# Kernel optimization log

Hardware: AMD Instinct MI355X
Metric: run time of the kernel (lower is better)

The kernel has to match this reference:

```python
import jax, jax.numpy as jnp
import numpy as np

B, S, D, NB = 64, 2048, 512, 8
MAX_BLOCK = 64  # block lengths drawn from [1, MAX_BLOCK)


def setup_inputs() -> dict:
    key = jax.random.key(0)
    k_h, k_c, k_w, k_len, k_sel = jax.random.split(key, 5)
    h = jax.random.normal(k_h, (B, D), dtype=jnp.float32)
    context = jax.random.normal(k_c, (B, S, D), dtype=jnp.float32)
    W = jax.random.normal(k_w, (D, D), dtype=jnp.float32) / np.sqrt(D)
    # block lengths >= 1 so the selected block softmax is never empty;
    # sum of all blocks + 1 <= NB*(MAX_BLOCK-1)+1 < S, so slices stay in range
    sub_seq_lengths = jax.random.randint(k_len, (B, NB), 1, MAX_BLOCK, dtype=jnp.int32)
    selected_block_idx = jax.random.randint(k_sel, (B,), 0, NB, dtype=jnp.int32)
    return {"h": h, "context": context, "W": W,
            "sub_seq_lengths": sub_seq_lengths,
            "selected_block_idx": selected_block_idx}


def reference(h, context, W, sub_seq_lengths, selected_block_idx):
    # attn[b,s] = context[b,s] . (W h[b])   (linear_in has no bias)
    target = h @ W.T                                  # [B, D]
    attn = jnp.einsum('bsd,bd->bs', context, target)  # [B, S]

    # per-sample selected-block boundaries: sc = sum(lengths[:idx]) + 1
    starts = jnp.cumsum(sub_seq_lengths, axis=1) - sub_seq_lengths  # exclusive cumsum [B, NB]
    b = jnp.arange(h.shape[0])
    sc = starts[b, selected_block_idx] + 1            # [B]
    L = sub_seq_lengths[b, selected_block_idx]        # [B]

    pos = jnp.arange(context.shape[1])[None, :]       # [1, S]
    in_block = (pos >= sc[:, None]) & (pos < (sc + L)[:, None])  # [B, S]

    # masked softmax restricted to the selected block (vectorized over batch)
    p = jax.nn.softmax(jnp.where(in_block, attn, -jnp.inf), axis=1)
    p = jnp.where(in_block, p, 0.0)
    weighted_context = jnp.einsum('bs,bsd->bd', p, context)  # [B, D]
    return weighted_context, attn
```

## Files before the change

### kernel.cpp

```cpp
#include <hip/hip_runtime.h>
#include <hip/hip_bf16.h>
#include <stdint.h>

#define BB   64
#define SS   2048
#define DD   512
#define NBLK 8

typedef unsigned short u16;
typedef unsigned int   u32;

__device__ __forceinline__ float lo2f(u32 u) {
    union { u32 i; float f; } v; v.i = u << 16; return v.f;
}
__device__ __forceinline__ float hi2f(u32 u) {
    union { u32 i; float f; } v; v.i = u & 0xffff0000u; return v.f;
}

template<bool BF16>
__device__ __forceinline__ void load8(const void* base, size_t off, float* o) {
    if (BF16) {
        const uint4 v = *(const uint4*)((const u16*)base + off);
        o[0]=lo2f(v.x); o[1]=hi2f(v.x); o[2]=lo2f(v.y); o[3]=hi2f(v.y);
        o[4]=lo2f(v.z); o[5]=hi2f(v.z); o[6]=lo2f(v.w); o[7]=hi2f(v.w);
    } else {
        const float4* p = (const float4*)((const float*)base + off);
        const float4 a = p[0], b = p[1];
        o[0]=a.x; o[1]=a.y; o[2]=a.z; o[3]=a.w;
        o[4]=b.x; o[5]=b.y; o[6]=b.z; o[7]=b.w;
    }
}

template<bool BF16>
__device__ __forceinline__ float load1(const void* base, size_t idx) {
    if (BF16) return lo2f(((const u16*)base)[idx]);
    else      return ((const float*)base)[idx];
}

template<bool BF16>
__device__ __forceinline__ void store_out(void* base, size_t idx, float v) {
    if (BF16) ((__hip_bfloat16*)base)[idx] = __float2bfloat16(v);
    else      ((float*)base)[idx] = v;
}

template<bool BF16, bool TGT_WS>
__device__ __forceinline__ void load_tgt8(const void* tgt, size_t off, float* o) {
    if (TGT_WS) {
        const float4* p = (const float4*)((const float*)tgt + off);
        const float4 a = p[0], b = p[1];
        o[0]=a.x; o[1]=a.y; o[2]=a.z; o[3]=a.w;
        o[4]=b.x; o[5]=b.y; o[6]=b.z; o[7]=b.w;
    } else {
        load8<BF16>(tgt, off, o);
    }
}
template<bool BF16, bool TGT_WS>
__device__ __forceinline__ void store_tgt(void* tgt, size_t idx, float v) {
    if (TGT_WS) ((float*)tgt)[idx] = v;
    else        store_out<BF16>(tgt, idx, v);
}

__device__ __forceinline__ float dot8f(const float* a, const float* t) {
    float acc = a[0] * t[0];
    #pragma unroll
    for (int i = 1; i < 8; ++i) acc = fmaf(a[i], t[i], acc);
    return acc;
}

__device__ __forceinline__ float wave_reduce_sum(float acc) {
    #pragma unroll
    for (int off = 32; off >= 1; off >>= 1)
        acc += __shfl_xor(acc, off, 64);
    return acc;
}

__global__ void k0_sniff(const u32* __restrict__ ctx_w, int* __restrict__ flag) {
    const int lane = threadIdx.x;
    const u32 w = ctx_w[(size_t)lane * 997];
    const u32 e = (w >> 7) & 0xFF;
    int ok = (e >= 100 && e <= 135) ? 1 : 0;
    #pragma unroll
    for (int off = 32; off >= 1; off >>= 1)
        ok += __shfl_xor(ok, off, 64);
    if (lane == 0) *flag = (ok >= 32) ? 1 : 0;
}

#define K1_IPW 4
template<bool BF16, bool TGT_WS>
__global__ __launch_bounds__(256) void k1_target(
        const void* __restrict__ h, const void* __restrict__ W,
        void* __restrict__ tgt, const int* __restrict__ flag) {
    if ((*flag != 0) != BF16) return;
    const int wid  = (blockIdx.x * blockDim.x + threadIdx.x) >> 6;
    const int lane = threadIdx.x & 63;
    const int out0 = wid * K1_IPW;
    const int b    = out0 / DD;
    const int i0   = out0 - b * DD;

    float hf[8];
    load8<BF16>(h, (size_t)b * DD + lane * 8, hf);

    #pragma unroll
    for (int r = 0; r < K1_IPW; ++r) {
        const int i = i0 + r;
        float wf[8];
        load8<BF16>(W, (size_t)i * DD + lane * 8, wf);
        float acc = dot8f(wf, hf);
        acc = wave_reduce_sum(acc);
        if (lane == 0) store_tgt<BF16, TGT_WS>(tgt, (size_t)b * DD + i, acc);
    }
}

#define K2_RPW 8
template<bool BF16, bool TGT_WS>
__global__ __launch_bounds__(256) void k2_attn(
        const void* __restrict__ ctx, const void* __restrict__ tgt,
        void* __restrict__ dout, const int* __restrict__ flag) {
    if ((*flag != 0) != BF16) return;
    void* attn_out = BF16 ? (void*)((u16*)dout + (size_t)BB * DD)
                          : (void*)((float*)dout + (size_t)BB * DD);

    const int wid  = (blockIdx.x * blockDim.x + threadIdx.x) >> 6;
    const int lane = threadIdx.x & 63;
    const size_t row0 = (size_t)wid * K2_RPW;
    const int b = (int)(row0 >> 11);

    float t[8];
    load_tgt8<BF16, TGT_WS>(tgt, (size_t)b * DD + lane * 8, t);

    const size_t cbase = row0 * DD + (size_t)lane * 8;
    float keep = 0.f;
    #pragma unroll
    for (int r = 0; r < K2_RPW; ++r) {
        float cf[8];
        load8<BF16>(ctx, cbase + (size_t)r * DD, cf);
        float acc = dot8f(cf, t);
        acc = wave_reduce_sum(acc);
        if (lane == r) keep = acc;
    }
    if (lane < K2_RPW)
        store_out<BF16>(attn_out, row0 + lane, keep);
}

template<bool BF16, bool TGT_WS>
__global__ __launch_bounds__(256) void k3_softmax_wc(
        const void* __restrict__ ctx, const void* __restrict__ tgt,
        const int* __restrict__ lens, const int* __restrict__ sel,
        void* __restrict__ dout, const int* __restrict__ flag) {
    if ((*flag != 0) != BF16) return;
    const int b    = blockIdx.x;
    const int tid  = threadIdx.x;
    const int lane = tid & 63;
    const int wave = tid >> 6;

    __shared__ float attn_s[64];
    __shared__ float p_s[64];

    const int sidx = sel[b];
    int start = 0;
    #pragma unroll
    for (int j = 0; j < NBLK; ++j) {
        int lj = lens[b * NBLK + j];
        if (j < sidx) start += lj;
    }
    const int L  = lens[b * NBLK + sidx];
    const int sc = start + 1;

    float t[8];
    load_tgt8<BF16, TGT_WS>(tgt, (size_t)b * DD + lane * 8, t);

    for (int s = wave; s < L; s += 4) {
        float cf[8];
        load8<BF16>(ctx, ((size_t)b * SS + sc + s) * DD + lane * 8, cf);
        float acc = dot8f(cf, t);
        acc = wave_reduce_sum(acc);
        if (lane == 0) attn_s[s] = acc;
    }
    __syncthreads();

    if (tid < 64) {
        const float v = (tid < L) ? attn_s[tid] : -INFINITY;
        float m = v;
        #pragma unroll
        for (int off = 32; off >= 1; off >>= 1)
            m = fmaxf(m, __shfl_xor(m, off, 64));
        const float e = (tid < L) ? __expf(v - m) : 0.f;
        float sum = e;
        #pragma unroll
        for (int off = 32; off >= 1; off >>= 1)
            sum += __shfl_xor(sum, off, 64);
        p_s[tid] = e / sum;
    }
    __syncthreads();

    #pragma unroll
    for (int rep = 0; rep < 2; ++rep) {
        const int d = tid + rep * 256;
        float acc = 0.f;
        for (int s = 0; s < L; ++s)
            acc = fmaf(p_s[s], load1<BF16>(ctx, ((size_t)b * SS + sc + s) * DD + d), acc);
        store_out<BF16>(dout, (size_t)b * DD + d, acc);
    }
}

extern "C" void kernel_launch(void* const* d_in, const int* in_sizes, int n_in,
                              void* d_out, int out_size, void* d_ws, size_t ws_size,
                              hipStream_t stream) {
    const void* h    = d_in[0];
    const void* ctx  = d_in[1];
    const void* W    = d_in[2];
    const int* lens  = (const int*)d_in[3];
    const int* sel   = (const int*)d_in[4];

    int* flag = (int*)d_ws;
    float* tgt_ws = (float*)((char*)d_ws + 256);
    const bool use_ws = (ws_size >= 256 + (size_t)BB * DD * 4);

    k0_sniff<<<1, 64, 0, stream>>>((const u32*)ctx, flag);

    const int g1 = (BB * DD / K1_IPW) / 4;
    const int g2 = (BB * SS / K2_RPW) / 4;

    if (use_ws) {
        k1_target<true , true ><<<g1, 256, 0, stream>>>(h, W, tgt_ws, flag);
        k1_target<false, true ><<<g1, 256, 0, stream>>>(h, W, tgt_ws, flag);
        k2_attn  <true , true ><<<g2, 256, 0, stream>>>(ctx, tgt_ws, d_out, flag);
        k2_attn  <false, true ><<<g2, 256, 0, stream>>>(ctx, tgt_ws, d_out, flag);
        k3_softmax_wc<true , true ><<<BB, 256, 0, stream>>>(ctx, tgt_ws, lens, sel, d_out, flag);
        k3_softmax_wc<false, true ><<<BB, 256, 0, stream>>>(ctx, tgt_ws, lens, sel, d_out, flag);
    } else {
        k1_target<true , false><<<g1, 256, 0, stream>>>(h, W, d_out, flag);
        k1_target<false, false><<<g1, 256, 0, stream>>>(h, W, d_out, flag);
        k2_attn  <true , false><<<g2, 256, 0, stream>>>(ctx, d_out, d_out, flag);
        k2_attn  <false, false><<<g2, 256, 0, stream>>>(ctx, d_out, d_out, flag);
        k3_softmax_wc<true , false><<<BB, 256, 0, stream>>>(ctx, d_out, lens, sel, d_out, flag);
        k3_softmax_wc<false, false><<<BB, 256, 0, stream>>>(ctx, d_out, lens, sel, d_out, flag);
    }
}
```

Measured before the change: 385.3 us.

## Drop dtype sniffing, specialize to fp32, batch wave reductions, vectorize weighted sum

Removes the runtime dtype-sniff kernel and the duplicated bf16/fp32 launches, so only three fp32 kernels run. The per-row full wave reductions in the target and attention kernels become a transpose-style butterfly reduction that reduces several partial sums together with fewer shuffles. The weighted-context stage now reads context rows with float4 loads split across waves and combines the waves through shared memory, replacing strided scalar loads. In exchange the bf16 input path is dropped, so the kernel assumes fp32 inputs.

```diff
diff --git a/kernel.cpp b/kernel.cpp
--- a/kernel.cpp
+++ b/kernel.cpp
@@ -7,57 +7,11 @@
 #define DD   512
 #define NBLK 8
 
-typedef unsigned short u16;
-typedef unsigned int   u32;
-
-__device__ __forceinline__ float lo2f(u32 u) {
-    union { u32 i; float f; } v; v.i = u << 16; return v.f;
-}
-__device__ __forceinline__ float hi2f(u32 u) {
-    union { u32 i; float f; } v; v.i = u & 0xffff0000u; return v.f;
-}
-
-template<bool BF16>
-__device__ __forceinline__ void load8(const void* base, size_t off, float* o) {
-    if (BF16) {
-        const uint4 v = *(const uint4*)((const u16*)base + off);
-        o[0]=lo2f(v.x); o[1]=hi2f(v.x); o[2]=lo2f(v.y); o[3]=hi2f(v.y);
-        o[4]=lo2f(v.z); o[5]=hi2f(v.z); o[6]=lo2f(v.w); o[7]=hi2f(v.w);
-    } else {
-        const float4* p = (const float4*)((const float*)base + off);
-        const float4 a = p[0], b = p[1];
-        o[0]=a.x; o[1]=a.y; o[2]=a.z; o[3]=a.w;
-        o[4]=b.x; o[5]=b.y; o[6]=b.z; o[7]=b.w;
-    }
-}
-
-template<bool BF16>
-__device__ __forceinline__ float load1(const void* base, size_t idx) {
-    if (BF16) return lo2f(((const u16*)base)[idx]);
-    else      return ((const float*)base)[idx];
-}
-
-template<bool BF16>
-__device__ __forceinline__ void store_out(void* base, size_t idx, float v) {
-    if (BF16) ((__hip_bfloat16*)base)[idx] = __float2bfloat16(v);
-    else      ((float*)base)[idx] = v;
-}
-
-template<bool BF16, bool TGT_WS>
-__device__ __forceinline__ void load_tgt8(const void* tgt, size_t off, float* o) {
-    if (TGT_WS) {
-        const float4* p = (const float4*)((const float*)tgt + off);
-        const float4 a = p[0], b = p[1];
-        o[0]=a.x; o[1]=a.y; o[2]=a.z; o[3]=a.w;
-        o[4]=b.x; o[5]=b.y; o[6]=b.z; o[7]=b.w;
-    } else {
-        load8<BF16>(tgt, off, o);
-    }
-}
-template<bool BF16, bool TGT_WS>
-__device__ __forceinline__ void store_tgt(void* tgt, size_t idx, float v) {
-    if (TGT_WS) ((float*)tgt)[idx] = v;
-    else        store_out<BF16>(tgt, idx, v);
+__device__ __forceinline__ void load8f(const float* __restrict__ p, float* o) {
+    const float4 a = ((const float4*)p)[0];
+    const float4 b = ((const float4*)p)[1];
+    o[0]=a.x; o[1]=a.y; o[2]=a.z; o[3]=a.w;
+    o[4]=b.x; o[5]=b.y; o[6]=b.z; o[7]=b.w;
 }
 
 __device__ __forceinline__ float dot8f(const float* a, const float* t) {
@@ -74,23 +28,10 @@
     return acc;
 }
 
-__global__ void k0_sniff(const u32* __restrict__ ctx_w, int* __restrict__ flag) {
-    const int lane = threadIdx.x;
-    const u32 w = ctx_w[(size_t)lane * 997];
-    const u32 e = (w >> 7) & 0xFF;
-    int ok = (e >= 100 && e <= 135) ? 1 : 0;
-    #pragma unroll
-    for (int off = 32; off >= 1; off >>= 1)
-        ok += __shfl_xor(ok, off, 64);
-    if (lane == 0) *flag = (ok >= 32) ? 1 : 0;
-}
-
 #define K1_IPW 4
-template<bool BF16, bool TGT_WS>
-__global__ __launch_bounds__(256) void k1_target(
-        const void* __restrict__ h, const void* __restrict__ W,
-        void* __restrict__ tgt, const int* __restrict__ flag) {
-    if ((*flag != 0) != BF16) return;
+__global__ __launch_bounds__(256) void sdba_k1_target(
+        const float* __restrict__ h, const float* __restrict__ W,
+        float* __restrict__ tgt) {
     const int wid  = (blockIdx.x * blockDim.x + threadIdx.x) >> 6;
     const int lane = threadIdx.x & 63;
     const int out0 = wid * K1_IPW;
@@ -98,56 +39,102 @@
     const int i0   = out0 - b * DD;
 
     float hf[8];
-    load8<BF16>(h, (size_t)b * DD + lane * 8, hf);
-
+    load8f(h + (size_t)b * DD + lane * 8, hf);
+
+    float acc[K1_IPW];
     #pragma unroll
     for (int r = 0; r < K1_IPW; ++r) {
-        const int i = i0 + r;
         float wf[8];
-        load8<BF16>(W, (size_t)i * DD + lane * 8, wf);
-        float acc = dot8f(wf, hf);
-        acc = wave_reduce_sum(acc);
-        if (lane == 0) store_tgt<BF16, TGT_WS>(tgt, (size_t)b * DD + i, acc);
-    }
+        load8f(W + (size_t)(i0 + r) * DD + lane * 8, wf);
+        acc[r] = dot8f(wf, hf);
+    }
+
+    float b2[2];
+    {
+        const int bit = lane & 1;
+        #pragma unroll
+        for (int j = 0; j < 2; ++j) {
+            float keep = bit ? acc[2*j+1] : acc[2*j];
+            float send = bit ? acc[2*j]   : acc[2*j+1];
+            b2[j] = keep + __shfl_xor(send, 1, 64);
+        }
+    }
+    float v;
+    {
+        const int bit = (lane >> 1) & 1;
+        float keep = bit ? b2[1] : b2[0];
+        float send = bit ? b2[0] : b2[1];
+        v = keep + __shfl_xor(send, 2, 64);
+    }
+    v += __shfl_xor(v, 4, 64);
+    v += __shfl_xor(v, 8, 64);
+    v += __shfl_xor(v, 16, 64);
+    v += __shfl_xor(v, 32, 64);
+
+    if (lane < K1_IPW)
+        tgt[(size_t)out0 + lane] = v;
 }
 
 #define K2_RPW 8
-template<bool BF16, bool TGT_WS>
-__global__ __launch_bounds__(256) void k2_attn(
-        const void* __restrict__ ctx, const void* __restrict__ tgt,
-        void* __restrict__ dout, const int* __restrict__ flag) {
-    if ((*flag != 0) != BF16) return;
-    void* attn_out = BF16 ? (void*)((u16*)dout + (size_t)BB * DD)
-                          : (void*)((float*)dout + (size_t)BB * DD);
-
+__global__ __launch_bounds__(256) void sdba_k2_attn(
+        const float* __restrict__ ctx, const float* __restrict__ tgt,
+        float* __restrict__ attn_out) {
     const int wid  = (blockIdx.x * blockDim.x + threadIdx.x) >> 6;
     const int lane = threadIdx.x & 63;
     const size_t row0 = (size_t)wid * K2_RPW;
     const int b = (int)(row0 >> 11);
 
     float t[8];
-    load_tgt8<BF16, TGT_WS>(tgt, (size_t)b * DD + lane * 8, t);
-
-    const size_t cbase = row0 * DD + (size_t)lane * 8;
-    float keep = 0.f;
+    load8f(tgt + (size_t)b * DD + lane * 8, t);
+
+    const float* cbase = ctx + row0 * DD + (size_t)lane * 8;
+    float acc[K2_RPW];
     #pragma unroll
     for (int r = 0; r < K2_RPW; ++r) {
         float cf[8];
-        load8<BF16>(ctx, cbase + (size_t)r * DD, cf);
-        float acc = dot8f(cf, t);
-        acc = wave_reduce_sum(acc);
-        if (lane == r) keep = acc;
-    }
+        load8f(cbase + (size_t)r * DD, cf);
+        acc[r] = dot8f(cf, t);
+    }
+
+    float b4[4];
+    {
+        const int bit = lane & 1;
+        #pragma unroll
+        for (int j = 0; j < 4; ++j) {
+            float keep = bit ? acc[2*j+1] : acc[2*j];
+            float send = bit ? acc[2*j]   : acc[2*j+1];
+            b4[j] = keep + __shfl_xor(send, 1, 64);
+        }
+    }
+    float b2[2];
+    {
+        const int bit = (lane >> 1) & 1;
+        #pragma unroll
+        for (int j = 0; j < 2; ++j) {
+            float keep = bit ? b4[2*j+1] : b4[2*j];
+            float send = bit ? b4[2*j]   : b4[2*j+1];
+            b2[j] = keep + __shfl_xor(send, 2, 64);
+        }
+    }
+    float v;
+    {
+        const int bit = (lane >> 2) & 1;
+        float keep = bit ? b2[1] : b2[0];
+        float send = bit ? b2[0] : b2[1];
+        v = keep + __shfl_xor(send, 4, 64);
+    }
+    v += __shfl_xor(v, 8, 64);
+    v += __shfl_xor(v, 16, 64);
+    v += __shfl_xor(v, 32, 64);
+
     if (lane < K2_RPW)
-        store_out<BF16>(attn_out, row0 + lane, keep);
-}
-
-template<bool BF16, bool TGT_WS>
-__global__ __launch_bounds__(256) void k3_softmax_wc(
-        const void* __restrict__ ctx, const void* __restrict__ tgt,
+        attn_out[row0 + lane] = v;
+}
+
+__global__ __launch_bounds__(256) void sdba_k3_softmax_wc(
+        const float* __restrict__ ctx, const float* __restrict__ tgt,
         const int* __restrict__ lens, const int* __restrict__ sel,
-        void* __restrict__ dout, const int* __restrict__ flag) {
-    if ((*flag != 0) != BF16) return;
+        float* __restrict__ out_wc) {
     const int b    = blockIdx.x;
     const int tid  = threadIdx.x;
     const int lane = tid & 63;
@@ -155,6 +142,7 @@
 
     __shared__ float attn_s[64];
     __shared__ float p_s[64];
+    __shared__ float red[4][DD];
 
     const int sidx = sel[b];
     int start = 0;
@@ -167,11 +155,11 @@
     const int sc = start + 1;
 
     float t[8];
-    load_tgt8<BF16, TGT_WS>(tgt, (size_t)b * DD + lane * 8, t);
+    load8f(tgt + (size_t)b * DD + lane * 8, t);
 
     for (int s = wave; s < L; s += 4) {
         float cf[8];
-        load8<BF16>(ctx, ((size_t)b * SS + sc + s) * DD + lane * 8, cf);
+        load8f(ctx + ((size_t)b * SS + sc + s) * DD + lane * 8, cf);
         float acc = dot8f(cf, t);
         acc = wave_reduce_sum(acc);
         if (lane == 0) attn_s[s] = acc;
@@ -193,47 +181,46 @@
     }
     __syncthreads();
 
+    float acc[8] = {0,0,0,0,0,0,0,0};
+    for (int s = wave; s < L; s += 4) {
+        float cf[8];
+        load8f(ctx + ((size_t)b * SS + sc + s) * DD + lane * 8, cf);
+        const float ps = p_s[s];
+        #pragma unroll
+        for (int j = 0; j < 8; ++j)
+            acc[j] = fmaf(ps, cf[j], acc[j]);
+    }
+    #pragma unroll
+    for (int j = 0; j < 8; ++j)
+        red[wave][lane * 8 + j] = acc[j];
+    __syncthreads();
+
     #pragma unroll
     for (int rep = 0; rep < 2; ++rep) {
         const int d = tid + rep * 256;
-        float acc = 0.f;
-        for (int s = 0; s < L; ++s)
-            acc = fmaf(p_s[s], load1<BF16>(ctx, ((size_t)b * SS + sc + s) * DD + d), acc);
-        store_out<BF16>(dout, (size_t)b * DD + d, acc);
+        const float v = red[0][d] + red[1][d] + red[2][d] + red[3][d];
+        out_wc[(size_t)b * DD + d] = v;
     }
 }
 
 extern "C" void kernel_launch(void* const* d_in, const int* in_sizes, int n_in,
                               void* d_out, int out_size, void* d_ws, size_t ws_size,
                               hipStream_t stream) {
-    const void* h    = d_in[0];
-    const void* ctx  = d_in[1];
-    const void* W    = d_in[2];
+    const float* h   = (const float*)d_in[0];
+    const float* ctx = (const float*)d_in[1];
+    const float* W   = (const float*)d_in[2];
     const int* lens  = (const int*)d_in[3];
     const int* sel   = (const int*)d_in[4];
 
-    int* flag = (int*)d_ws;
-    float* tgt_ws = (float*)((char*)d_ws + 256);
-    const bool use_ws = (ws_size >= 256 + (size_t)BB * DD * 4);
-
-    k0_sniff<<<1, 64, 0, stream>>>((const u32*)ctx, flag);
+    float* out      = (float*)d_out;
+    float* attn_out = out + (size_t)BB * DD;
+
+    float* tgt = (ws_size >= (size_t)BB * DD * 4) ? (float*)d_ws : out;
 
     const int g1 = (BB * DD / K1_IPW) / 4;
     const int g2 = (BB * SS / K2_RPW) / 4;
 
-    if (use_ws) {
-        k1_target<true , true ><<<g1, 256, 0, stream>>>(h, W, tgt_ws, flag);
-        k1_target<false, true ><<<g1, 256, 0, stream>>>(h, W, tgt_ws, flag);
-        k2_attn  <true , true ><<<g2, 256, 0, stream>>>(ctx, tgt_ws, d_out, flag);
-        k2_attn  <false, true ><<<g2, 256, 0, stream>>>(ctx, tgt_ws, d_out, flag);
-        k3_softmax_wc<true , true ><<<BB, 256, 0, stream>>>(ctx, tgt_ws, lens, sel, d_out, flag);
-        k3_softmax_wc<false, true ><<<BB, 256, 0, stream>>>(ctx, tgt_ws, lens, sel, d_out, flag);
-    } else {
-        k1_target<true , false><<<g1, 256, 0, stream>>>(h, W, d_out, flag);
-        k1_target<false, false><<<g1, 256, 0, stream>>>(h, W, d_out, flag);
-        k2_attn  <true , false><<<g2, 256, 0, stream>>>(ctx, d_out, d_out, flag);
-        k2_attn  <false, false><<<g2, 256, 0, stream>>>(ctx, d_out, d_out, flag);
-        k3_softmax_wc<true , false><<<BB, 256, 0, stream>>>(ctx, d_out, lens, sel, d_out, flag);
-        k3_softmax_wc<false, false><<<BB, 256, 0, stream>>>(ctx, d_out, lens, sel, d_out, flag);
-    }
-}
+    sdba_k1_target<<<g1, 256, 0, stream>>>(h, W, tgt);
+    sdba_k2_attn<<<g2, 256, 0, stream>>>(ctx, tgt, attn_out);
+    sdba_k3_softmax_wc<<<BB, 256, 0, stream>>>(ctx, tgt, lens, sel, out);
+}
```

New measurement: 377.5 us. 1.02x faster.
